# Performance work log

Measured on AMD Instinct MI355X. Metric: run time of the kernel, lower is better.

The kernel has to match this reference:

```python
import jax, jax.numpy as jnp
import numpy as np

N_NODES = 100000
N_EDGES = 1600000
IN_DIM = 256
OUT_DIM = 128
EPS = 1e-12  # torch F.normalize default eps


def setup_inputs() -> dict:
    key = jax.random.key(0)
    k1, k2, k3, k4, k5 = jax.random.split(key, 5)
    x = jax.random.normal(k1, (N_NODES, IN_DIM), dtype=jnp.float32)
    edge_index = jax.random.randint(k2, (2, N_EDGES), 0, N_NODES, dtype=jnp.int64)
    # projection (no bias): weight [out, in]
    Wp = jax.random.normal(k3, (OUT_DIM, IN_DIM), dtype=jnp.float32) * 0.05
    # GCNConv internal linear weight [out, out] and output bias [out]
    Wg = jax.random.normal(k4, (OUT_DIM, OUT_DIM), dtype=jnp.float32) * 0.05
    bg = jax.random.normal(k5, (OUT_DIM,), dtype=jnp.float32) * 0.01
    return {"x": x, "edge_index": edge_index, "Wp": Wp, "Wg": Wg, "bg": bg}


def reference(x, edge_index, Wp, Wg, bg):
    n = x.shape[0]
    # projection: x @ Wp^T
    h = x @ Wp.T                      # [N, OUT]
    # GCNConv: transform first, then propagate
    h = h @ Wg.T                      # [N, OUT]
    # add self-loops
    loops = jnp.arange(n, dtype=edge_index.dtype)
    row = jnp.concatenate([edge_index[0], loops])   # source
    col = jnp.concatenate([edge_index[1], loops])   # target
    # symmetric normalization: deg over target index (edge_weight = 1)
    deg = jax.ops.segment_sum(jnp.ones_like(col, dtype=h.dtype), col, num_segments=n)
    dinv = jnp.where(deg > 0, jax.lax.rsqrt(deg), 0.0)
    norm = dinv[row] * dinv[col]                     # [E+N]
    # gather messages from source, scale, scatter-add to target
    msg = h[row] * norm[:, None]                     # [E+N, OUT]
    out = jax.ops.segment_sum(msg, col, num_segments=n)  # [N, OUT]
    out = out + bg
    # F.normalize(dim=1): divide by L2 norm clamped at eps
    nrm = jnp.sqrt(jnp.sum(out * out, axis=1, keepdims=True))
    out = out / jnp.maximum(nrm, EPS)
    return out
```

## Files before the change

### kernel.cpp

```cpp
#include <hip/hip_runtime.h>
#include <hip/hip_fp16.h>

#define NDIM 128
#define KDIM 256
#define MT 5
#define AROW 264
#define CHUNK 3200
#define BSH 9
#define BMASK 511
#define MAXBUCK 256

typedef _Float16 half8 __attribute__((ext_vector_type(8)));
typedef _Float16 half4v __attribute__((ext_vector_type(4)));
typedef float float4v __attribute__((ext_vector_type(4)));

__global__ void k_combine_w(const float* __restrict__ Wp, const float* __restrict__ Wg,
                            _Float16* __restrict__ Bfrag) {
    int o = blockIdx.x;
    int i = threadIdx.x;
    float acc = 0.f;
#pragma unroll 4
    for (int k = 0; k < 128; ++k) acc = fmaf(Wg[o * 128 + k], Wp[k * 256 + i], acc);
    int kk = i >> 5, r = i & 31, quad = r >> 3, j = r & 7;
    int ntile = o >> 4, lanen = o & 15, lane = quad * 16 + lanen;
    Bfrag[(((ntile * 8 + kk) * 64) + lane) * 8 + j] = (_Float16)acc;
}

__global__ __launch_bounds__(256) void k_phase1(const int* __restrict__ col, int E,
                                                int* __restrict__ hist, int NBLK, int NBUCK) {
    __shared__ int h[MAXBUCK];
    int tid = threadIdx.x;
    h[tid] = 0;
    __syncthreads();
    int e0 = blockIdx.x * CHUNK;
    int e1 = min(e0 + CHUNK, E);
    for (int e = e0 + tid; e < e1; e += 256) atomicAdd(&h[col[e] >> BSH], 1);
    __syncthreads();
    if (tid < NBUCK) hist[tid * NBLK + blockIdx.x] = h[tid];
}

__global__ __launch_bounds__(1024) void k_scan_blk(int* __restrict__ a, int n,
                                                   int* __restrict__ blockSum) {
    __shared__ int s[1024];
    int t = threadIdx.x;
    int i = blockIdx.x * 1024 + t;
    int v = (i < n) ? a[i] : 0;
    s[t] = v;
    __syncthreads();
    for (int d = 1; d < 1024; d <<= 1) {
        int y = (t >= d) ? s[t - d] : 0;
        __syncthreads();
        s[t] += y;
        __syncthreads();
    }
    if (i < n) a[i] = s[t] - v;
    if (t == 1023) blockSum[blockIdx.x] = s[t];
}

__global__ __launch_bounds__(1024) void k_scan_top(int* __restrict__ blockSum, int nb) {
    __shared__ int s[1024];
    int t = threadIdx.x;
    int v = (t < nb) ? blockSum[t] : 0;
    s[t] = v;
    __syncthreads();
    for (int d = 1; d < 1024; d <<= 1) {
        int y = (t >= d) ? s[t - d] : 0;
        __syncthreads();
        s[t] += y;
        __syncthreads();
    }
    if (t < nb) blockSum[t] = s[t] - v;
}

__global__ __launch_bounds__(256) void k_scan_add(int* __restrict__ a,
                                                  const int* __restrict__ blockOff, int n) {
    int i = blockIdx.x * 256 + threadIdx.x;
    if (i < n) a[i] += blockOff[i >> 10];
}

__global__ __launch_bounds__(256) void k_phase3(const int* __restrict__ ei, int E,
                                                const int* __restrict__ offs, int NBLK, int NBUCK,
                                                int* __restrict__ tmp) {
    __shared__ int cur[MAXBUCK];
    int tid = threadIdx.x;
    if (tid < NBUCK) cur[tid] = offs[tid * NBLK + blockIdx.x];
    __syncthreads();
    int e0 = blockIdx.x * CHUNK;
    int e1 = min(e0 + CHUNK, E);
    for (int e = e0 + tid; e < e1; e += 256) {
        int r = ei[e];
        int c = ei[E + e];
        int p = atomicAdd(&cur[c >> BSH], 1);
        tmp[p] = (r << BSH) | (c & BMASK);
    }
}

__global__ __launch_bounds__(512) void k_fine(const int* __restrict__ tmp,
                                              const int* __restrict__ offs, int NBLK, int NBUCK,
                                              int N, int E,
                                              int* __restrict__ sortedRow,
                                              int* __restrict__ cnt,
                                              int* __restrict__ rowStart) {
    __shared__ int scnt[512];
    __shared__ int cur[512];
    int b = blockIdx.x;
    int t = threadIdx.x;
    int start = offs[b * NBLK];
    int end = (b + 1 < NBUCK) ? offs[(b + 1) * NBLK] : E;

    scnt[t] = 0;
    __syncthreads();
    for (int p = start + t; p < end; p += 512) atomicAdd(&scnt[tmp[p] & BMASK], 1);
    __syncthreads();
    int v = scnt[t];
    for (int d = 1; d < 512; d <<= 1) {
        int y = (t >= d) ? scnt[t - d] : 0;
        __syncthreads();
        scnt[t] += y;
        __syncthreads();
    }
    int excl = scnt[t] - v;
    int node = (b << BSH) + t;
    if (node < N) {
        cnt[node] = v;
        rowStart[node] = start + excl;
    }
    cur[t] = start + excl;
    __syncthreads();
    for (int p = start + t; p < end; p += 512) {
        int pr = tmp[p];
        int slot = atomicAdd(&cur[pr & BMASK], 1);
        sortedRow[slot] = pr >> BSH;
    }
    if (b == NBUCK - 1 && t == 0) rowStart[N] = E;
}

__global__ __launch_bounds__(256) void k_gemm_mfma(const float* __restrict__ x,
                                                   const _Float16* __restrict__ Bfrag,
                                                   const int* __restrict__ cnt,
                                                   _Float16* __restrict__ g, int nrows) {
    __shared__ __align__(16) _Float16 xs[2][16 * AROW];
    int tid  = threadIdx.x;
    int lane = tid & 63;
    int w    = tid >> 6;
    int quad = lane >> 4;
    int lcol = lane & 15;

    const half8* Bv = (const half8*)Bfrag;
    half8 b0[8], b1[8];
#pragma unroll
    for (int kk = 0; kk < 8; ++kk) {
        b0[kk] = Bv[(w * 8 + kk) * 64 + lane];
        b1[kk] = Bv[((w + 4) * 8 + kk) * 64 + lane];
    }

    long base = (long)blockIdx.x * (16 * MT);
    for (int t = 0; t < MT; ++t) {
        long m0 = base + t * 16;
        _Float16* xb = xs[t & 1];
        const float4* xv = (const float4*)(x + m0 * KDIM);
#pragma unroll
        for (int ii = 0; ii < 4; ++ii) {
            int idx = tid + ii * 256;
            int m = idx >> 6, k4 = idx & 63;
            float4 v = xv[idx];
            half4v hv = { (_Float16)v.x, (_Float16)v.y, (_Float16)v.z, (_Float16)v.w };
            *(half4v*)&xb[m * AROW + k4 * 4] = hv;
        }
        __syncthreads();

        float4v acc0 = {0.f, 0.f, 0.f, 0.f}, acc1 = {0.f, 0.f, 0.f, 0.f};
#pragma unroll
        for (int kk = 0; kk < 8; ++kk) {
            half8 a = *(const half8*)(&xb[lcol * AROW + kk * 32 + quad * 8]);
            acc0 = __builtin_amdgcn_mfma_f32_16x16x32_f16(a, b0[kk], acc0, 0, 0, 0);
            acc1 = __builtin_amdgcn_mfma_f32_16x16x32_f16(a, b1[kk], acc1, 0, 0, 0);
        }

#pragma unroll
        for (int r = 0; r < 4; ++r) {
            long node = m0 + quad * 4 + r;
            float di = rsqrtf((float)(cnt[node] + 1));
            g[node * NDIM + w * 16 + lcol]        = (_Float16)(acc0[r] * di);
            g[node * NDIM + (w + 4) * 16 + lcol]  = (_Float16)(acc1[r] * di);
        }
    }
}

__global__ __launch_bounds__(256) void k_gather(const _Float16* __restrict__ g,
                                                const int* __restrict__ rowStart,
                                                const int* __restrict__ sortedRow,
                                                const int* __restrict__ cnt,
                                                const float* __restrict__ bg,
                                                float* __restrict__ out) {
    int lane = threadIdx.x & 63;
    int i = blockIdx.x * 4 + (threadIdx.x >> 6);
    const int s = rowStart[i];
    const int e = rowStart[i + 1];
    const int g4  = lane >> 4;
    const int r16 = lane & 15;

    const half8* __restrict__ gv = (const half8*)g;

    float acc[8];
#pragma unroll
    for (int j = 0; j < 8; ++j) acc[j] = 0.f;

    int p = s;
    for (; p + 16 <= e; p += 16) {
        int r0 = sortedRow[p + g4];
        int r1 = sortedRow[p + 4 + g4];
        int r2 = sortedRow[p + 8 + g4];
        int r3 = sortedRow[p + 12 + g4];
        half8 v0 = gv[(size_t)r0 * 16 + r16];
        half8 v1 = gv[(size_t)r1 * 16 + r16];
        half8 v2 = gv[(size_t)r2 * 16 + r16];
        half8 v3 = gv[(size_t)r3 * 16 + r16];
#pragma unroll
        for (int j = 0; j < 8; ++j)
            acc[j] += ((float)v0[j] + (float)v1[j]) + ((float)v2[j] + (float)v3[j]);
    }
    for (; p + 4 <= e; p += 4) {
        int r0 = sortedRow[p + g4];
        half8 v0 = gv[(size_t)r0 * 16 + r16];
#pragma unroll
        for (int j = 0; j < 8; ++j) acc[j] += (float)v0[j];
    }
    if (p + g4 < e) {
        int r0 = sortedRow[p + g4];
        half8 v0 = gv[(size_t)r0 * 16 + r16];
#pragma unroll
        for (int j = 0; j < 8; ++j) acc[j] += (float)v0[j];
    }

#pragma unroll
    for (int j = 0; j < 8; ++j) {
        acc[j] += __shfl_xor(acc[j], 16);
        acc[j] += __shfl_xor(acc[j], 32);
    }

    half8 sv = gv[(size_t)i * 16 + r16];
#pragma unroll
    for (int j = 0; j < 8; ++j) acc[j] += (float)sv[j];

    float di = rsqrtf((float)(cnt[i] + 1));
    float4 b0 = ((const float4*)bg)[r16 * 2];
    float4 b1 = ((const float4*)bg)[r16 * 2 + 1];
    float v[8];
    v[0] = fmaf(di, acc[0], b0.x);
    v[1] = fmaf(di, acc[1], b0.y);
    v[2] = fmaf(di, acc[2], b0.z);
    v[3] = fmaf(di, acc[3], b0.w);
    v[4] = fmaf(di, acc[4], b1.x);
    v[5] = fmaf(di, acc[5], b1.y);
    v[6] = fmaf(di, acc[6], b1.z);
    v[7] = fmaf(di, acc[7], b1.w);

    float sq = 0.f;
#pragma unroll
    for (int j = 0; j < 8; ++j) sq += v[j] * v[j];
    sq += __shfl_xor(sq, 1);
    sq += __shfl_xor(sq, 2);
    sq += __shfl_xor(sq, 4);
    sq += __shfl_xor(sq, 8);
    float scale = 1.0f / fmaxf(sqrtf(sq), 1e-12f);

    if (g4 == 0) {
        float4 o0 = make_float4(v[0] * scale, v[1] * scale, v[2] * scale, v[3] * scale);
        float4 o1 = make_float4(v[4] * scale, v[5] * scale, v[6] * scale, v[7] * scale);
        ((float4*)out)[(size_t)i * 32 + r16 * 2]     = o0;
        ((float4*)out)[(size_t)i * 32 + r16 * 2 + 1] = o1;
    }
}

extern "C" void kernel_launch(void* const* d_in, const int* in_sizes, int n_in,
                              void* d_out, int out_size, void* d_ws, size_t ws_size,
                              hipStream_t stream) {
    const float* x  = (const float*)d_in[0];
    const int*   ei = (const int*)  d_in[1];
    const float* Wp = (const float*)d_in[2];
    const float* Wg = (const float*)d_in[3];
    const float* bg = (const float*)d_in[4];
    float* out = (float*)d_out;

    const int N = in_sizes[0] / KDIM;
    const int E = in_sizes[1] / 2;

    const int NBLK  = (E + CHUNK - 1) / CHUNK;
    const int NBUCK = (N + BMASK) >> BSH;
    const int NE    = NBLK * NBUCK;
    const int NSB   = (NE + 1023) >> 10;

    char* p = (char*)d_ws;
    auto carve = [&](size_t bytes) { void* r = (void*)p; p += (bytes + 255) & ~(size_t)255; return r; };
    _Float16* g      = (_Float16*)carve((size_t)N * NDIM * 2);
    int*   sortedRow = (int*)  carve((size_t)E * 4);
    int*   tmp       = (int*)  carve((size_t)E * 4);
    _Float16* Bfrag  = (_Float16*)carve((size_t)KDIM * NDIM * 2);
    int*   cnt       = (int*)  carve((size_t)N * 4);
    int*   rowStart  = (int*)  carve((size_t)(N + 1) * 4);
    int*   hist      = (int*)  carve((size_t)NE * 4);
    int*   blockSum  = (int*)  carve((size_t)1024 * 4);

    hipLaunchKernelGGL(k_combine_w, dim3(NDIM), dim3(KDIM), 0, stream, Wp, Wg, Bfrag);
    hipLaunchKernelGGL(k_phase1, dim3(NBLK), dim3(256), 0, stream, ei + E, E, hist, NBLK, NBUCK);
    hipLaunchKernelGGL(k_scan_blk, dim3(NSB), dim3(1024), 0, stream, hist, NE, blockSum);
    hipLaunchKernelGGL(k_scan_top, dim3(1), dim3(1024), 0, stream, blockSum, NSB);
    hipLaunchKernelGGL(k_scan_add, dim3((NE + 255) / 256), dim3(256), 0, stream, hist, blockSum, NE);
    hipLaunchKernelGGL(k_phase3, dim3(NBLK), dim3(256), 0, stream, ei, E, hist, NBLK, NBUCK, tmp);
    hipLaunchKernelGGL(k_fine, dim3(NBUCK), dim3(512), 0, stream, tmp, hist, NBLK, NBUCK, N, E,
                       sortedRow, cnt, rowStart);
    hipLaunchKernelGGL(k_gemm_mfma, dim3(N / (16 * MT)), dim3(256), 0, stream, x, Bfrag, cnt, g, N);
    hipLaunchKernelGGL(k_gather, dim3(N / 4), dim3(256), 0, stream,
                       g, rowStart, sortedRow, cnt, bg, out);
}
```

Before: 307.3 us.

## Fuse CSR build into one cooperative kernel with grid-wide syncs

Replaces the six-kernel CSR construction (histogram, three-stage scan, scatter, fine sort) with a single cooperative kernel of 1024 blocks that uses grid.sync between phases. Buckets become 256 nodes wide, so each bucket is fine-sorted by one 256-thread block. The aim is to remove per-launch overhead and the gaps between small kernels. In exchange it depends on cooperative launch succeeding (falling back to the old path otherwise), pays for grid barriers, and uses a differently sized histogram.

```diff
diff --git a/kernel.cpp b/kernel.cpp
--- a/kernel.cpp
+++ b/kernel.cpp
@@ -1,14 +1,22 @@
 #include <hip/hip_runtime.h>
 #include <hip/hip_fp16.h>
+#include <hip/hip_cooperative_groups.h>
+
+namespace cg = cooperative_groups;
 
 #define NDIM 128
 #define KDIM 256
 #define MT 5
 #define AROW 264
+
 #define CHUNK 3200
 #define BSH 9
 #define BMASK 511
 #define MAXBUCK 256
+
+#define CNBLK 1024
+#define CBSH 8
+#define CBMASK 255
 
 typedef _Float16 half8 __attribute__((ext_vector_type(8)));
 typedef _Float16 half4v __attribute__((ext_vector_type(4)));
@@ -24,6 +32,125 @@
     int kk = i >> 5, r = i & 31, quad = r >> 3, j = r & 7;
     int ntile = o >> 4, lanen = o & 15, lane = quad * 16 + lanen;
     Bfrag[(((ntile * 8 + kk) * 64) + lane) * 8 + j] = (_Float16)acc;
+}
+
+__global__ __launch_bounds__(256) void k_csr(const int* __restrict__ ei, int E, int N,
+                                             int* __restrict__ tmp,
+                                             int* __restrict__ sortedRow,
+                                             int* __restrict__ cnt,
+                                             int* __restrict__ rowStart,
+                                             int* __restrict__ hist,
+                                             int* __restrict__ blockSum) {
+    cg::grid_group grid = cg::this_grid();
+    __shared__ int sh[512];
+    __shared__ int sh2[512];
+    const int tid = threadIdx.x;
+    const int blk = blockIdx.x;
+    const int NBUCK = (N + CBMASK) >> CBSH;
+    const int NE = NBUCK * CNBLK;
+    const int SCCH = (NE + CNBLK - 1) / CNBLK;
+    const int ECH = (E + CNBLK - 1) / CNBLK;
+    const int e0 = blk * ECH;
+    const int e1 = min(e0 + ECH, E);
+    const int* __restrict__ col = ei + E;
+
+    sh[tid] = 0; sh[tid + 256] = 0;
+    __syncthreads();
+    for (int e = e0 + tid; e < e1; e += 256) atomicAdd(&sh[col[e] >> CBSH], 1);
+    __syncthreads();
+    for (int b = tid; b < NBUCK; b += 256) hist[b * CNBLK + blk] = sh[b];
+
+    grid.sync();
+
+    {
+        int base = blk * SCCH;
+        int lim = min(SCCH, NE - base);
+        int i0 = base + tid * 2;
+        int v0 = (tid * 2     < lim) ? hist[i0]     : 0;
+        int v1 = (tid * 2 + 1 < lim) ? hist[i0 + 1] : 0;
+        int mysum = v0 + v1;
+        sh[tid] = mysum;
+        __syncthreads();
+        for (int d = 1; d < 256; d <<= 1) {
+            int y = (tid >= d) ? sh[tid - d] : 0;
+            __syncthreads();
+            sh[tid] += y;
+            __syncthreads();
+        }
+        int excl = sh[tid] - mysum;
+        if (tid * 2     < lim) hist[i0]     = excl;
+        if (tid * 2 + 1 < lim) hist[i0 + 1] = excl + v0;
+        if (tid == 255) blockSum[blk] = sh[255];
+    }
+
+    grid.sync();
+
+    if (blk == 0) {
+        int b0 = tid * 4;
+        int w0 = blockSum[b0], w1 = blockSum[b0 + 1], w2 = blockSum[b0 + 2], w3 = blockSum[b0 + 3];
+        int mysum = w0 + w1 + w2 + w3;
+        sh[tid] = mysum;
+        __syncthreads();
+        for (int d = 1; d < 256; d <<= 1) {
+            int y = (tid >= d) ? sh[tid - d] : 0;
+            __syncthreads();
+            sh[tid] += y;
+            __syncthreads();
+        }
+        int excl = sh[tid] - mysum;
+        blockSum[b0]     = excl;
+        blockSum[b0 + 1] = excl + w0;
+        blockSum[b0 + 2] = excl + w0 + w1;
+        blockSum[b0 + 3] = excl + w0 + w1 + w2;
+    }
+
+    grid.sync();
+
+    for (int b = tid; b < NBUCK; b += 256) {
+        int idx = b * CNBLK + blk;
+        sh2[b] = hist[idx] + blockSum[idx / SCCH];
+    }
+    __syncthreads();
+    for (int e = e0 + tid; e < e1; e += 256) {
+        int r = ei[e];
+        int c = col[e];
+        int p = atomicAdd(&sh2[c >> CBSH], 1);
+        tmp[p] = (r << CBSH) | (c & CBMASK);
+    }
+
+    grid.sync();
+
+    if (blk < NBUCK) {
+        int i0 = blk * CNBLK;
+        int start = hist[i0] + blockSum[i0 / SCCH];
+        int end = (blk + 1 < NBUCK)
+                    ? (hist[i0 + CNBLK] + blockSum[(i0 + CNBLK) / SCCH]) : E;
+        sh[tid] = 0;
+        __syncthreads();
+        for (int p = start + tid; p < end; p += 256) atomicAdd(&sh[tmp[p] & CBMASK], 1);
+        __syncthreads();
+        int v = sh[tid];
+        for (int d = 1; d < 256; d <<= 1) {
+            int y = (tid >= d) ? sh[tid - d] : 0;
+            __syncthreads();
+            sh[tid] += y;
+            __syncthreads();
+        }
+        int excl = sh[tid] - v;
+        int node = (blk << CBSH) + tid;
+        if (node < N) {
+            cnt[node] = v;
+            rowStart[node] = start + excl;
+        }
+        sh2[tid] = start + excl;
+        __syncthreads();
+        for (int p = start + tid; p < end; p += 256) {
+            int pr = tmp[p];
+            int slot = atomicAdd(&sh2[pr & CBMASK], 1);
+            sortedRow[slot] = pr >> CBSH;
+        }
+        if (blk == 0 && tid == 0) rowStart[N] = E;
+    }
 }
 
 __global__ __launch_bounds__(256) void k_phase1(const int* __restrict__ col, int E,
@@ -286,10 +413,15 @@
     const int N = in_sizes[0] / KDIM;
     const int E = in_sizes[1] / 2;
 
+    const int CNBUCK = (N + CBMASK) >> CBSH;
+    const int CNE    = CNBUCK * CNBLK;
+
     const int NBLK  = (E + CHUNK - 1) / CHUNK;
     const int NBUCK = (N + BMASK) >> BSH;
     const int NE    = NBLK * NBUCK;
     const int NSB   = (NE + 1023) >> 10;
+
+    const int histN = (CNE > NE) ? CNE : NE;
 
     char* p = (char*)d_ws;
     auto carve = [&](size_t bytes) { void* r = (void*)p; p += (bytes + 255) & ~(size_t)255; return r; };
@@ -299,17 +431,30 @@
     _Float16* Bfrag  = (_Float16*)carve((size_t)KDIM * NDIM * 2);
     int*   cnt       = (int*)  carve((size_t)N * 4);
     int*   rowStart  = (int*)  carve((size_t)(N + 1) * 4);
-    int*   hist      = (int*)  carve((size_t)NE * 4);
+    int*   hist      = (int*)  carve((size_t)histN * 4);
     int*   blockSum  = (int*)  carve((size_t)1024 * 4);
 
     hipLaunchKernelGGL(k_combine_w, dim3(NDIM), dim3(KDIM), 0, stream, Wp, Wg, Bfrag);
-    hipLaunchKernelGGL(k_phase1, dim3(NBLK), dim3(256), 0, stream, ei + E, E, hist, NBLK, NBUCK);
-    hipLaunchKernelGGL(k_scan_blk, dim3(NSB), dim3(1024), 0, stream, hist, NE, blockSum);
-    hipLaunchKernelGGL(k_scan_top, dim3(1), dim3(1024), 0, stream, blockSum, NSB);
-    hipLaunchKernelGGL(k_scan_add, dim3((NE + 255) / 256), dim3(256), 0, stream, hist, blockSum, NE);
-    hipLaunchKernelGGL(k_phase3, dim3(NBLK), dim3(256), 0, stream, ei, E, hist, NBLK, NBUCK, tmp);
-    hipLaunchKernelGGL(k_fine, dim3(NBUCK), dim3(512), 0, stream, tmp, hist, NBLK, NBUCK, N, E,
-                       sortedRow, cnt, rowStart);
+
+    {
+        const int* eiA = ei; int Ev = E, Nv = N;
+        int* tmpA = tmp; int* srA = sortedRow; int* cntA = cnt; int* rsA = rowStart;
+        int* histA = hist; int* bsA = blockSum;
+        void* cargs[] = { (void*)&eiA, (void*)&Ev, (void*)&Nv, (void*)&tmpA, (void*)&srA,
+                          (void*)&cntA, (void*)&rsA, (void*)&histA, (void*)&bsA };
+        hipError_t cerr = hipLaunchCooperativeKernel((void*)k_csr, dim3(CNBLK), dim3(256),
+                                                     cargs, 0, stream);
+        if (cerr != hipSuccess) {
+            hipLaunchKernelGGL(k_phase1, dim3(NBLK), dim3(256), 0, stream, ei + E, E, hist, NBLK, NBUCK);
+            hipLaunchKernelGGL(k_scan_blk, dim3(NSB), dim3(1024), 0, stream, hist, NE, blockSum);
+            hipLaunchKernelGGL(k_scan_top, dim3(1), dim3(1024), 0, stream, blockSum, NSB);
+            hipLaunchKernelGGL(k_scan_add, dim3((NE + 255) / 256), dim3(256), 0, stream, hist, blockSum, NE);
+            hipLaunchKernelGGL(k_phase3, dim3(NBLK), dim3(256), 0, stream, ei, E, hist, NBLK, NBUCK, tmp);
+            hipLaunchKernelGGL(k_fine, dim3(NBUCK), dim3(512), 0, stream, tmp, hist, NBLK, NBUCK, N, E,
+                               sortedRow, cnt, rowStart);
+        }
+    }
+
     hipLaunchKernelGGL(k_gemm_mfma, dim3(N / (16 * MT)), dim3(256), 0, stream, x, Bfrag, cnt, g, N);
     hipLaunchKernelGGL(k_gather, dim3(N / 4), dim3(256), 0, stream,
                        g, rowStart, sortedRow, cnt, bg, out);
```

Result: slower. 776.7 us (+152.8%).

## Use finer sort buckets and fdot2-based fp16 accumulation in gather

Applied to the files above, without the earlier changes.

Bucket width in the two-level counting sort drops from 512 to 256 nodes, giving about 391 buckets and so more fine-sort blocks with fewer edges each. The bucket loops in the histogram and scatter kernels are generalized to handle more buckets than threads. The gather kernel now sums fp16 pairs with the fdot2 builtin against a ones vector, cutting the number of conversions and adds. It also adds an 8-edge tail step, which shortens the remainder loop. The fdot2 path accumulates pairs through a dot instruction, which may round slightly differently, and the larger histogram adds a little scan work.

```diff
diff --git a/kernel.cpp b/kernel.cpp
--- a/kernel.cpp
+++ b/kernel.cpp
@@ -6,13 +6,21 @@
 #define MT 5
 #define AROW 264
 #define CHUNK 3200
-#define BSH 9
-#define BMASK 511
-#define MAXBUCK 256
+#define BSH 8
+#define BMASK 255
+#define MAXBUCK 400
+#define FTH 512
 
 typedef _Float16 half8 __attribute__((ext_vector_type(8)));
 typedef _Float16 half4v __attribute__((ext_vector_type(4)));
+typedef _Float16 half2v __attribute__((ext_vector_type(2)));
 typedef float float4v __attribute__((ext_vector_type(4)));
+
+#if __has_builtin(__builtin_amdgcn_fdot2)
+#define HAS_FDOT2 1
+#else
+#define HAS_FDOT2 0
+#endif
 
 __global__ void k_combine_w(const float* __restrict__ Wp, const float* __restrict__ Wg,
                             _Float16* __restrict__ Bfrag) {
@@ -30,13 +38,13 @@
                                                 int* __restrict__ hist, int NBLK, int NBUCK) {
     __shared__ int h[MAXBUCK];
     int tid = threadIdx.x;
-    h[tid] = 0;
+    for (int b = tid; b < MAXBUCK; b += 256) h[b] = 0;
     __syncthreads();
     int e0 = blockIdx.x * CHUNK;
     int e1 = min(e0 + CHUNK, E);
     for (int e = e0 + tid; e < e1; e += 256) atomicAdd(&h[col[e] >> BSH], 1);
     __syncthreads();
-    if (tid < NBUCK) hist[tid * NBLK + blockIdx.x] = h[tid];
+    for (int b = tid; b < NBUCK; b += 256) hist[b * NBLK + blockIdx.x] = h[b];
 }
 
 __global__ __launch_bounds__(1024) void k_scan_blk(int* __restrict__ a, int n,
@@ -83,7 +91,7 @@
                                                 int* __restrict__ tmp) {
     __shared__ int cur[MAXBUCK];
     int tid = threadIdx.x;
-    if (tid < NBUCK) cur[tid] = offs[tid * NBLK + blockIdx.x];
+    for (int b = tid; b < NBUCK; b += 256) cur[b] = offs[b * NBLK + blockIdx.x];
     __syncthreads();
     int e0 = blockIdx.x * CHUNK;
     int e1 = min(e0 + CHUNK, E);
@@ -95,39 +103,41 @@
     }
 }
 
-__global__ __launch_bounds__(512) void k_fine(const int* __restrict__ tmp,
+__global__ __launch_bounds__(FTH) void k_fine(const int* __restrict__ tmp,
                                               const int* __restrict__ offs, int NBLK, int NBUCK,
                                               int N, int E,
                                               int* __restrict__ sortedRow,
                                               int* __restrict__ cnt,
                                               int* __restrict__ rowStart) {
-    __shared__ int scnt[512];
-    __shared__ int cur[512];
+    __shared__ int scnt[256];
+    __shared__ int cur[256];
     int b = blockIdx.x;
     int t = threadIdx.x;
     int start = offs[b * NBLK];
     int end = (b + 1 < NBUCK) ? offs[(b + 1) * NBLK] : E;
 
-    scnt[t] = 0;
-    __syncthreads();
-    for (int p = start + t; p < end; p += 512) atomicAdd(&scnt[tmp[p] & BMASK], 1);
-    __syncthreads();
-    int v = scnt[t];
-    for (int d = 1; d < 512; d <<= 1) {
-        int y = (t >= d) ? scnt[t - d] : 0;
-        __syncthreads();
-        scnt[t] += y;
-        __syncthreads();
-    }
-    int excl = scnt[t] - v;
-    int node = (b << BSH) + t;
-    if (node < N) {
-        cnt[node] = v;
-        rowStart[node] = start + excl;
-    }
-    cur[t] = start + excl;
-    __syncthreads();
-    for (int p = start + t; p < end; p += 512) {
+    if (t < 256) scnt[t] = 0;
+    __syncthreads();
+    for (int p = start + t; p < end; p += FTH) atomicAdd(&scnt[tmp[p] & BMASK], 1);
+    __syncthreads();
+    int v = (t < 256) ? scnt[t] : 0;
+    for (int d = 1; d < 256; d <<= 1) {
+        int y = (t >= d && t < 256) ? scnt[t - d] : 0;
+        __syncthreads();
+        if (t < 256) scnt[t] += y;
+        __syncthreads();
+    }
+    if (t < 256) {
+        int excl = scnt[t] - v;
+        int node = (b << BSH) + t;
+        if (node < N) {
+            cnt[node] = v;
+            rowStart[node] = start + excl;
+        }
+        cur[t] = start + excl;
+    }
+    __syncthreads();
+    for (int p = start + t; p < end; p += FTH) {
         int pr = tmp[p];
         int slot = atomicAdd(&cur[pr & BMASK], 1);
         sortedRow[slot] = pr >> BSH;
@@ -206,6 +216,10 @@
 #pragma unroll
     for (int j = 0; j < 8; ++j) acc[j] = 0.f;
 
+#if HAS_FDOT2
+    const half2v one2 = { (_Float16)1.0f, (_Float16)1.0f };
+#endif
+
     int p = s;
     for (; p + 16 <= e; p += 16) {
         int r0 = sortedRow[p + g4];
@@ -216,15 +230,43 @@
         half8 v1 = gv[(size_t)r1 * 16 + r16];
         half8 v2 = gv[(size_t)r2 * 16 + r16];
         half8 v3 = gv[(size_t)r3 * 16 + r16];
+#if HAS_FDOT2
+#pragma unroll
+        for (int j = 0; j < 8; ++j) {
+            half2v a = { v0[j], v1[j] };
+            half2v b = { v2[j], v3[j] };
+            acc[j] = __builtin_amdgcn_fdot2(a, one2,
+                     __builtin_amdgcn_fdot2(b, one2, acc[j], false), false);
+        }
+#else
 #pragma unroll
         for (int j = 0; j < 8; ++j)
             acc[j] += ((float)v0[j] + (float)v1[j]) + ((float)v2[j] + (float)v3[j]);
-    }
-    for (; p + 4 <= e; p += 4) {
+#endif
+    }
+    if (p + 8 <= e) {
+        int r0 = sortedRow[p + g4];
+        int r1 = sortedRow[p + 4 + g4];
+        half8 v0 = gv[(size_t)r0 * 16 + r16];
+        half8 v1 = gv[(size_t)r1 * 16 + r16];
+#if HAS_FDOT2
+#pragma unroll
+        for (int j = 0; j < 8; ++j) {
+            half2v a = { v0[j], v1[j] };
+            acc[j] = __builtin_amdgcn_fdot2(a, one2, acc[j], false);
+        }
+#else
+#pragma unroll
+        for (int j = 0; j < 8; ++j) acc[j] += (float)v0[j] + (float)v1[j];
+#endif
+        p += 8;
+    }
+    if (p + 4 <= e) {
         int r0 = sortedRow[p + g4];
         half8 v0 = gv[(size_t)r0 * 16 + r16];
 #pragma unroll
         for (int j = 0; j < 8; ++j) acc[j] += (float)v0[j];
+        p += 4;
     }
     if (p + g4 < e) {
         int r0 = sortedRow[p + g4];
@@ -308,7 +350,7 @@
     hipLaunchKernelGGL(k_scan_top, dim3(1), dim3(1024), 0, stream, blockSum, NSB);
     hipLaunchKernelGGL(k_scan_add, dim3((NE + 255) / 256), dim3(256), 0, stream, hist, blockSum, NE);
     hipLaunchKernelGGL(k_phase3, dim3(NBLK), dim3(256), 0, stream, ei, E, hist, NBLK, NBUCK, tmp);
-    hipLaunchKernelGGL(k_fine, dim3(NBUCK), dim3(512), 0, stream, tmp, hist, NBLK, NBUCK, N, E,
+    hipLaunchKernelGGL(k_fine, dim3(NBUCK), dim3(FTH), 0, stream, tmp, hist, NBLK, NBUCK, N, E,
                        sortedRow, cnt, rowStart);
     hipLaunchKernelGGL(k_gemm_mfma, dim3(N / (16 * MT)), dim3(256), 0, stream, x, Bfrag, cnt, g, N);
     hipLaunchKernelGGL(k_gather, dim3(N / 4), dim3(256), 0, stream,
```

New measurement: 313.2 us. Within noise of the previous version (+1.9%).
